# Kernel optimization log

Measured on AMD Instinct MI355X. Metric: run time of the kernel, lower is better.

## Reference

```python
import jax, jax.numpy as jnp
import numpy as np

EPS = 1e-12

def _normalize(v):
    n = jnp.linalg.norm(v, axis=-1, keepdims=True)
    return v / jnp.maximum(n, EPS)

def _bgs(J):
    # J: [b, N, D, 3, 2] -> rotation matrices R [b, N, D, 3, 3]
    b1 = _normalize(J[..., :, 0])
    a2 = J[..., :, 1]
    dot = jnp.sum(b1 * a2, axis=-1, keepdims=True)
    b2 = _normalize(a2 - dot * b1)
    b3 = jnp.cross(b1, b2)
    return jnp.stack([b1, b2, b3], axis=-1)  # columns b1,b2,b3

def setup_inputs() -> dict:
    key = jax.random.key(0)
    k1, k2, k3, k4, k5 = jax.random.split(key, 5)
    B, N, D, OUT = 16, 4096, 64, 64
    X = jax.random.normal(k1, (B, N, D, 3), dtype=jnp.float32)
    J = jax.random.normal(k2, (B, N, D, 3, 2), dtype=jnp.float32)
    A = jax.random.normal(k3, (OUT, D), dtype=jnp.float32)
    Bm = jax.random.normal(k4, (OUT, D), dtype=jnp.float32)
    C = jax.random.normal(k5, (OUT, D), dtype=jnp.float32)
    return {"X": X, "J": J, "A": A, "Bm": Bm, "C": C}

def reference(X, J, A, Bm, C):
    R = _bgs(J)  # [b, N, D, 3, 3]
    # RT_i . X == column i of R dotted with X -> scalar per channel
    RTX = jnp.einsum('bndij,bndi->bndj', R, X)  # [b, N, D, 3], j-th entry = RT_j X
    rt0 = RTX[..., 0:1]
    rt1 = RTX[..., 1:2]
    rt2 = RTX[..., 2:3]
    col0 = R[..., :, 0]
    col1 = R[..., :, 1]
    col2 = R[..., :, 2]
    # a_term (after adding b_term, as in original forward)
    a_term = col1 * rt1 + col2 * rt2 + col2 * rt1 - col1 * rt2  # [b, N, D, 3]
    c_term = col0 * rt0
    Y = jnp.einsum('fe,bnei->bnfi', A, a_term) + jnp.einsum('fe,bnei->bnfi', C, c_term)
    Y = jnp.einsum('fe,bnei->bnfi', Bm, Y)
    return Y
```

## Files before the change

kernel.cpp:

```cpp
#include <hip/hip_runtime.h>


typedef __bf16 bf16x8 __attribute__((ext_vector_type(8)));
typedef float floatx4 __attribute__((ext_vector_type(4)));

#define RSW 68

__global__ __launch_bounds__(64) void prep_kernel(const float* __restrict__ A,
                                                  const float* __restrict__ Bm,
                                                  const float* __restrict__ C,
                                                  __bf16* __restrict__ acat) {
    int tid = blockIdx.x * 64 + threadIdx.x;
    int f = tid >> 6;
    int e = tid & 63;
    float m = 0.f, m2 = 0.f;
    #pragma unroll 8
    for (int k = 0; k < 64; ++k) {
        float b = Bm[f * 64 + k];
        m  = fmaf(b, A[k * 64 + e], m);
        m2 = fmaf(b, C[k * 64 + e], m2);
    }
    acat[f * 128 + 2 * e]     = (__bf16)m;
    acat[f * 128 + 2 * e + 1] = (__bf16)m2;
}

static __device__ __forceinline__ unsigned pk(float a, float c) {
    unsigned short ua = __builtin_bit_cast(unsigned short, (__bf16)a);
    unsigned short uc = __builtin_bit_cast(unsigned short, (__bf16)c);
    return ((unsigned)uc << 16) | ua;
}

__global__ __launch_bounds__(256, 4) void main_kernel(const float* __restrict__ X,
                                                      const float* __restrict__ J,
                                                      const __bf16* __restrict__ acat,
                                                      float* __restrict__ out) {
    __shared__ __align__(16) float buf[4][2304];

    const int wave = threadIdx.x >> 6;
    const int lane = threadIdx.x & 63;
    const int l15  = lane & 15;
    const int quad = lane >> 4;
    const int pbase = blockIdx.x * 16 + wave * 4;

    float* stg = buf[wave];

    {
        const floatx4* jg = (const floatx4*)(J + (size_t)pbase * 384);
        const floatx4* xg = (const floatx4*)(X + (size_t)pbase * 192);
        floatx4 jt[6], xt[3];
        #pragma unroll
        for (int t = 0; t < 6; ++t) jt[t] = jg[t * 64 + lane];
        #pragma unroll
        for (int t = 0; t < 3; ++t) xt[t] = xg[t * 64 + lane];
        floatx4* sj = (floatx4*)stg;
        floatx4* sx = (floatx4*)(stg + 1536);
        #pragma unroll
        for (int t = 0; t < 6; ++t) sj[t * 64 + lane] = jt[t];
        #pragma unroll
        for (int t = 0; t < 3; ++t) sx[t * 64 + lane] = xt[t];
    }

    __asm__ volatile("s_waitcnt lgkmcnt(0)" ::: "memory");

    float2 ja, jb, jc; float xx, xy, xz;
    {
        const float* jst = stg + lane * 6;
        ja = *(const float2*)(jst);
        jb = *(const float2*)(jst + 2);
        jc = *(const float2*)(jst + 4);
        const float* xst = stg + 1536 + lane * 3;
        xx = xst[0]; xy = xst[1]; xz = xst[2];
    }
    #pragma unroll
    for (int pi = 0; pi < 4; ++pi) {
        float2 na = ja, nb = jb, nc = jc; float nx = xx, ny = xy, nz = xz;
        if (pi < 3) {
            const float* jst = stg + (pi + 1) * 384 + lane * 6;
            na = *(const float2*)(jst);
            nb = *(const float2*)(jst + 2);
            nc = *(const float2*)(jst + 4);
            const float* xst = stg + 1536 + (pi + 1) * 192 + lane * 3;
            nx = xst[0]; ny = xst[1]; nz = xst[2];
        }

        float a0x = ja.x, a0y = jb.x, a0z = jc.x;
        float a1x = ja.y, a1y = jb.y, a1z = jc.y;

        float n0 = sqrtf(a0x * a0x + a0y * a0y + a0z * a0z);
        float r0 = 1.0f / fmaxf(n0, 1e-12f);
        float b1x = a0x * r0, b1y = a0y * r0, b1z = a0z * r0;

        float d  = b1x * a1x + b1y * a1y + b1z * a1z;
        float ux = a1x - d * b1x, uy = a1y - d * b1y, uz = a1z - d * b1z;
        float n2 = sqrtf(ux * ux + uy * uy + uz * uz);
        float r2 = 1.0f / fmaxf(n2, 1e-12f);
        float b2x = ux * r2, b2y = uy * r2, b2z = uz * r2;

        float b3x = b1y * b2z - b1z * b2y;
        float b3y = b1z * b2x - b1x * b2z;
        float b3z = b1x * b2y - b1y * b2x;

        float rt0 = b1x * xx + b1y * xy + b1z * xz;
        float rt1 = b2x * xx + b2y * xy + b2z * xz;
        float rt2 = b3x * xx + b3y * xy + b3z * xz;

        float s = rt1 - rt2, tt = rt1 + rt2;

        unsigned* zr = (unsigned*)(stg + pi * 396);
        zr[lane]           = pk(b2x * s + b3x * tt, b1x * rt0);
        zr[RSW + lane]     = pk(b2y * s + b3y * tt, b1y * rt0);
        zr[2 * RSW + lane] = pk(b2z * s + b3z * tt, b1z * rt0);

        ja = na; jb = nb; jc = nc; xx = nx; xy = ny; xz = nz;
    }

    bf16x8 afrag[4][4];
    #pragma unroll
    for (int mt = 0; mt < 4; ++mt)
        #pragma unroll
        for (int kc = 0; kc < 4; ++kc)
            afrag[mt][kc] = *(const bf16x8*)(acat + (mt * 16 + l15) * 128 + kc * 32 + quad * 8);

    __asm__ volatile("s_waitcnt lgkmcnt(0)" ::: "memory");

    floatx4 acc[4];
    #pragma unroll
    for (int mt = 0; mt < 4; ++mt) acc[mt] = (floatx4){0.f, 0.f, 0.f, 0.f};

    int row = l15 > 11 ? 11 : l15;
    int pz  = (row * 21846) >> 16;
    int iz  = row - pz * 3;
    const __bf16* zb = (const __bf16*)stg + pz * 792 + iz * 136;
    #pragma unroll
    for (int kc = 0; kc < 4; ++kc) {
        bf16x8 b = *(const bf16x8*)(zb + kc * 32 + quad * 8);
        #pragma unroll
        for (int mt = 0; mt < 4; ++mt)
            acc[mt] = __builtin_amdgcn_mfma_f32_16x16x32_bf16(afrag[mt][kc], b, acc[mt], 0, 0, 0);
    }

    __asm__ volatile("s_waitcnt lgkmcnt(0)" ::: "memory");

    float* dl = stg;
    #pragma unroll
    for (int mt = 0; mt < 4; ++mt) {
        int n = l15;
        if (n < 12) {
            int pl = (n * 21846) >> 16;
            int i  = n - pl * 3;
            float* dst = dl + pl * 196 + i;
            #pragma unroll
            for (int r = 0; r < 4; ++r) {
                int f = mt * 16 + quad * 4 + r;
                dst[f * 3] = acc[mt][r];
            }
        }
    }

    __asm__ volatile("s_waitcnt lgkmcnt(0)" ::: "memory");

    floatx4* og = (floatx4*)(out + (size_t)pbase * 192);
    #pragma unroll
    for (int t = 0; t < 3; ++t) {
        int g  = t * 64 + lane;
        int pg = (g * 1366) >> 16;
        int o  = g - pg * 48;
        og[g] = *(const floatx4*)(dl + pg * 196 + o * 4);
    }
}

extern "C" void kernel_launch(void* const* d_in, const int* in_sizes, int n_in,
                              void* d_out, int out_size, void* d_ws, size_t ws_size,
                              hipStream_t stream) {
    const float* X  = (const float*)d_in[0];
    const float* J  = (const float*)d_in[1];
    const float* A  = (const float*)d_in[2];
    const float* Bm = (const float*)d_in[3];
    const float* C  = (const float*)d_in[4];
    float* out = (float*)d_out;
    __bf16* acat = (__bf16*)d_ws;

    prep_kernel<<<64, 64, 0, stream>>>(A, Bm, C, acat);

    main_kernel<<<4096, 256, 0, stream>>>(X, J, acat, out);
}
```

Before: 211.2 us.

## Load J/X directly to registers and stage shared weight matrix in swizzled LDS

Each lane now loads its J and X values straight from global memory into registers, dropping the LDS staging round-trip. The 64x128 bf16 combined weight matrix is loaded once per block cooperatively into LDS with an XOR swizzle, and MFMA A-fragments are read from LDS rather than each wave fetching them from global memory. This cuts per-wave global weight traffic and LDS staging, but adds a block-wide barrier and uncoalesced strided global loads for J/X. LDS use per block drops, which may allow more resident blocks.

```diff
diff --git a/kernel.cpp b/kernel.cpp
--- a/kernel.cpp
+++ b/kernel.cpp
@@ -4,7 +4,8 @@
 typedef __bf16 bf16x8 __attribute__((ext_vector_type(8)));
 typedef float floatx4 __attribute__((ext_vector_type(4)));
 
-#define RSW 68
+#define ZRS  68
+#define WLDS 816
 
 __global__ __launch_bounds__(64) void prep_kernel(const float* __restrict__ A,
                                                   const float* __restrict__ Bm,
@@ -34,57 +35,54 @@
                                                       const float* __restrict__ J,
                                                       const __bf16* __restrict__ acat,
                                                       float* __restrict__ out) {
-    __shared__ __align__(16) float buf[4][2304];
+    __shared__ __align__(16) float lds[4096 + 4 * WLDS];
 
-    const int wave = threadIdx.x >> 6;
-    const int lane = threadIdx.x & 63;
+    const int tid  = threadIdx.x;
+    const int wave = tid >> 6;
+    const int lane = tid & 63;
     const int l15  = lane & 15;
     const int quad = lane >> 4;
     const int pbase = blockIdx.x * 16 + wave * 4;
 
-    float* stg = buf[wave];
+    float2 jreg[4][3];
+    float  xreg[4][3];
+    {
+        const float* Jb = J + (size_t)pbase * 384 + lane * 6;
+        const float* Xb = X + (size_t)pbase * 192 + lane * 3;
+        #pragma unroll
+        for (int pi = 0; pi < 4; ++pi) {
+            jreg[pi][0] = *(const float2*)(Jb + pi * 384);
+            jreg[pi][1] = *(const float2*)(Jb + pi * 384 + 2);
+            jreg[pi][2] = *(const float2*)(Jb + pi * 384 + 4);
+            xreg[pi][0] = Xb[pi * 192];
+            xreg[pi][1] = Xb[pi * 192 + 1];
+            xreg[pi][2] = Xb[pi * 192 + 2];
+        }
+    }
 
     {
-        const floatx4* jg = (const floatx4*)(J + (size_t)pbase * 384);
-        const floatx4* xg = (const floatx4*)(X + (size_t)pbase * 192);
-        floatx4 jt[6], xt[3];
+        const floatx4* ag = (const floatx4*)acat;
+        floatx4 t[4];
         #pragma unroll
-        for (int t = 0; t < 6; ++t) jt[t] = jg[t * 64 + lane];
+        for (int u = 0; u < 4; ++u) t[u] = ag[u * 256 + tid];
         #pragma unroll
-        for (int t = 0; t < 3; ++t) xt[t] = xg[t * 64 + lane];
-        floatx4* sj = (floatx4*)stg;
-        floatx4* sx = (floatx4*)(stg + 1536);
-        #pragma unroll
-        for (int t = 0; t < 6; ++t) sj[t * 64 + lane] = jt[t];
-        #pragma unroll
-        for (int t = 0; t < 3; ++t) sx[t * 64 + lane] = xt[t];
+        for (int u = 0; u < 4; ++u) {
+            int Ld  = (u * 256 + tid) * 4;
+            int row = Ld >> 6;
+            int dst = Ld ^ ((row & 7) << 2);
+            *(floatx4*)(lds + dst) = t[u];
+        }
     }
+    __syncthreads();
 
-    __asm__ volatile("s_waitcnt lgkmcnt(0)" ::: "memory");
+    float* zbase = lds + 4096 + wave * WLDS;
 
-    float2 ja, jb, jc; float xx, xy, xz;
-    {
-        const float* jst = stg + lane * 6;
-        ja = *(const float2*)(jst);
-        jb = *(const float2*)(jst + 2);
-        jc = *(const float2*)(jst + 4);
-        const float* xst = stg + 1536 + lane * 3;
-        xx = xst[0]; xy = xst[1]; xz = xst[2];
-    }
     #pragma unroll
     for (int pi = 0; pi < 4; ++pi) {
-        float2 na = ja, nb = jb, nc = jc; float nx = xx, ny = xy, nz = xz;
-        if (pi < 3) {
-            const float* jst = stg + (pi + 1) * 384 + lane * 6;
-            na = *(const float2*)(jst);
-            nb = *(const float2*)(jst + 2);
-            nc = *(const float2*)(jst + 4);
-            const float* xst = stg + 1536 + (pi + 1) * 192 + lane * 3;
-            nx = xst[0]; ny = xst[1]; nz = xst[2];
-        }
-
-        float a0x = ja.x, a0y = jb.x, a0z = jc.x;
-        float a1x = ja.y, a1y = jb.y, a1z = jc.y;
+        float a0x = jreg[pi][0].x, a1x = jreg[pi][0].y;
+        float a0y = jreg[pi][1].x, a1y = jreg[pi][1].y;
+        float a0z = jreg[pi][2].x, a1z = jreg[pi][2].y;
+        float xx = xreg[pi][0], xy = xreg[pi][1], xz = xreg[pi][2];
 
         float n0 = sqrtf(a0x * a0x + a0y * a0y + a0z * a0z);
         float r0 = 1.0f / fmaxf(n0, 1e-12f);
@@ -106,20 +104,11 @@
 
         float s = rt1 - rt2, tt = rt1 + rt2;
 
-        unsigned* zr = (unsigned*)(stg + pi * 396);
+        unsigned* zr = (unsigned*)zbase + pi * (3 * ZRS);
         zr[lane]           = pk(b2x * s + b3x * tt, b1x * rt0);
-        zr[RSW + lane]     = pk(b2y * s + b3y * tt, b1y * rt0);
-        zr[2 * RSW + lane] = pk(b2z * s + b3z * tt, b1z * rt0);
-
-        ja = na; jb = nb; jc = nc; xx = nx; xy = ny; xz = nz;
+        zr[ZRS + lane]     = pk(b2y * s + b3y * tt, b1y * rt0);
+        zr[2 * ZRS + lane] = pk(b2z * s + b3z * tt, b1z * rt0);
     }
-
-    bf16x8 afrag[4][4];
-    #pragma unroll
-    for (int mt = 0; mt < 4; ++mt)
-        #pragma unroll
-        for (int kc = 0; kc < 4; ++kc)
-            afrag[mt][kc] = *(const bf16x8*)(acat + (mt * 16 + l15) * 128 + kc * 32 + quad * 8);
 
     __asm__ volatile("s_waitcnt lgkmcnt(0)" ::: "memory");
 
@@ -130,18 +119,23 @@
     int row = l15 > 11 ? 11 : l15;
     int pz  = (row * 21846) >> 16;
     int iz  = row - pz * 3;
-    const __bf16* zb = (const __bf16*)stg + pz * 792 + iz * 136;
+    const __bf16* zb = (const __bf16*)zbase + pz * (3 * ZRS * 2) + iz * (ZRS * 2);
+    const int sw = (l15 & 7) << 2;
     #pragma unroll
     for (int kc = 0; kc < 4; ++kc) {
         bf16x8 b = *(const bf16x8*)(zb + kc * 32 + quad * 8);
         #pragma unroll
-        for (int mt = 0; mt < 4; ++mt)
-            acc[mt] = __builtin_amdgcn_mfma_f32_16x16x32_bf16(afrag[mt][kc], b, acc[mt], 0, 0, 0);
+        for (int mt = 0; mt < 4; ++mt) {
+            int r   = mt * 16 + l15;
+            int off = r * 64 + ((kc * 16 + quad * 4) ^ sw);
+            bf16x8 a = *(const bf16x8*)((const __bf16*)lds + off * 2);
+            acc[mt] = __builtin_amdgcn_mfma_f32_16x16x32_bf16(a, b, acc[mt], 0, 0, 0);
+        }
     }
 
     __asm__ volatile("s_waitcnt lgkmcnt(0)" ::: "memory");
 
-    float* dl = stg;
+    float* dl = zbase;
     #pragma unroll
     for (int mt = 0; mt < 4; ++mt) {
         int n = l15;
```

Measured after the change: 204.8 us. -3.0%, faster.
